# Optimization experiments

Measured on AMD Instinct MI355X. Metric: run time of the kernel, lower is better.

## Reference

```python
import jax, jax.numpy as jnp
import numpy as np
from jax import lax

B, N, C = 8, 16384, 96
ROPE_BASE = 10000.0


def _rope(x):
    """Faithful port of the module's RoPE. x: (b, h, w, c).
    Note: the original computes angles over the h axis but, due to torch
    broadcasting of (h, k_max) against (b, h, w, k_max), the rotation is
    applied along the w axis (valid since h == w)."""
    b, h, w, c = x.shape
    k_max = c // 2
    theta = 1.0 / (ROPE_BASE ** (jnp.arange(k_max, dtype=x.dtype) / k_max))  # (k_max,)
    angles = jnp.arange(h, dtype=x.dtype)[:, None] * theta                  # (h, k_max)
    cos = jnp.cos(angles)[None, None, :, :]  # broadcast over w axis
    sin = jnp.sin(angles)[None, None, :, :]
    xr = x.reshape(b, h, w, k_max, 2)
    xre, xim = xr[..., 0], xr[..., 1]
    ore = xre * cos - xim * sin
    oim = xre * sin + xim * cos
    return jnp.stack([ore, oim], axis=-1).reshape(b, h, w, c)


def setup_inputs() -> dict:
    key = jax.random.key(0)
    ks = jax.random.split(key, 5)
    return {
        "x": jax.random.normal(ks[0], (B, N, C), dtype=jnp.float32),
        "qk_w": jax.random.normal(ks[1], (2 * C, C), dtype=jnp.float32) * 0.05,
        "qk_b": jax.random.normal(ks[2], (2 * C,), dtype=jnp.float32) * 0.02,
        "lepe_w": jax.random.normal(ks[3], (C, 1, 3, 3), dtype=jnp.float32) * 0.1,
        "lepe_b": jax.random.normal(ks[4], (C,), dtype=jnp.float32) * 0.02,
        "num_heads": 4,
    }


def reference(x, qk_w, qk_b, lepe_w, lepe_b, num_heads):
    b, n, c = x.shape
    h = w = int(round(n ** 0.5))
    d = c // num_heads
    inv_sqrt_n = float(n) ** (-0.5)

    qk = x @ qk_w.T + qk_b                        # (b, n, 2c)
    q = jax.nn.elu(qk[..., :c]) + 1.0             # (b, n, c)
    k = jax.nn.elu(qk[..., c:]) + 1.0
    v = x

    q_rope = _rope(q.reshape(b, h, w, c)).reshape(b, n, num_heads, d).transpose(0, 2, 1, 3)
    k_rope = _rope(k.reshape(b, h, w, c)).reshape(b, n, num_heads, d).transpose(0, 2, 1, 3)
    qh = q.reshape(b, n, num_heads, d).transpose(0, 2, 1, 3)  # (b, H, n, d)
    kh = k.reshape(b, n, num_heads, d).transpose(0, 2, 1, 3)
    vh = v.reshape(b, n, num_heads, d).transpose(0, 2, 1, 3)

    k_mean = kh.mean(axis=2, keepdims=True)                         # (b, H, 1, d)
    z = 1.0 / (jnp.einsum('bhnd,bhmd->bhnm', qh, k_mean) + 1e-6)    # (b, H, n, 1)
    kv = jnp.einsum('bhnd,bhne->bhde', k_rope * inv_sqrt_n, vh * inv_sqrt_n)  # (b, H, d, d)
    out = jnp.einsum('bhnd,bhde->bhne', q_rope, kv) * z             # (b, H, n, d)
    out = out.transpose(0, 2, 1, 3).reshape(b, n, c)

    # LePE: depthwise 3x3 conv on v laid out as (b, c, h, w)
    v_img = vh.transpose(0, 2, 1, 3).reshape(b, h, w, c).transpose(0, 3, 1, 2)
    lepe = lax.conv_general_dilated(
        v_img, lepe_w, window_strides=(1, 1), padding='SAME',
        feature_group_count=c, dimension_numbers=('NCHW', 'OIHW', 'NCHW'))
    lepe = lepe + lepe_b[None, :, None, None]
    return out + lepe.transpose(0, 2, 3, 1).reshape(b, n, c)
```

## Files before the change

kernel.cpp:

```cpp
#include <hip/hip_runtime.h>


#define NLINE 16384
#define CCH 96
#define KTP 136
#define QSP 104
#define OUTP 98
#define THETA_COEF 0.2768273412406135f
#define LOG2_2PI   2.6514961294723187f

typedef __attribute__((ext_vector_type(4))) float f32x4;
typedef __attribute__((ext_vector_type(8))) short bf16x8;
typedef __attribute__((ext_vector_type(2))) __fp16 fp16x2;

__device__ __forceinline__ unsigned short f2bf(float f) {
  unsigned int u = __float_as_uint(f);
  u += 0x7FFFu + ((u >> 16) & 1u);
  return (unsigned short)(u >> 16);
}
__device__ __forceinline__ float bf2f(unsigned short h) {
  return __uint_as_float(((unsigned int)h) << 16);
}
__device__ __forceinline__ bf16x8 pack_bf8(f32x4 v0, f32x4 v1) {
  bf16x8 r;
  r[0] = (short)f2bf(v0.x); r[1] = (short)f2bf(v0.y);
  r[2] = (short)f2bf(v0.z); r[3] = (short)f2bf(v0.w);
  r[4] = (short)f2bf(v1.x); r[5] = (short)f2bf(v1.y);
  r[6] = (short)f2bf(v1.z); r[7] = (short)f2bf(v1.w);
  return r;
}

__global__ void prep_w2(const float* __restrict__ qkw,
                        unsigned short* __restrict__ wfrag,
                        float* __restrict__ kv_g) {
  int idx = blockIdx.x * 256 + threadIdx.x;
  if (idx < 19200) kv_g[idx] = 0.0f;
  if (idx < 2304) {
    int u = idx;
    int lane = u & 63;
    int nt = (u >> 6) % 6;
    int rest = u / 384;
    int kk = rest % 3, half = rest / 3;
    int lr = lane & 15, q4 = lane >> 4;
    const float* src = qkw + (half * 96 + nt * 16 + lr) * 96 + kk * 32 + q4 * 8;
    unsigned short* dst = wfrag + (size_t)u * 8;
#pragma unroll
    for (int j = 0; j < 8; ++j) dst[j] = f2bf(src[j]);
  }
}

__global__ __launch_bounds__(256, 4) void la_k1(
    const float* __restrict__ x, const unsigned short* __restrict__ wfrag,
    const float* __restrict__ qkb, float* __restrict__ kv_g,
    float* __restrict__ ksum_g)
{
  const int tid  = threadIdx.x;
  const int b    = blockIdx.x >> 7;
  const int tile = blockIdx.x & 127;

  __shared__ alignas(16) unsigned short kqt[96 * KTP];
  __shared__ float ksum_s[96];

  if (tid < 96) ksum_s[tid] = 0.0f;
  __syncthreads();

  const int wave = tid >> 6;
  const int lane = tid & 63;
  const int lr   = lane & 15;
  const int q4   = lane >> 4;
  const int row0 = wave * 32;
  const float* xb = x + ((size_t)b * NLINE + (size_t)tile * 128) * CCH;

  bf16x8 afr[2][3];
#pragma unroll
  for (int mt = 0; mt < 2; ++mt)
#pragma unroll
    for (int kk = 0; kk < 3; ++kk) {
      const float* ap = xb + (row0 + mt * 16 + lr) * CCH + kk * 32 + q4 * 8;
      afr[mt][kk] = pack_bf8(((const f32x4*)ap)[0], ((const f32x4*)ap)[1]);
    }

  float biasv[6];
#pragma unroll
  for (int nt = 0; nt < 6; ++nt) biasv[nt] = qkb[96 + nt * 16 + lr];

  f32x4 acc[2][6];
#pragma unroll
  for (int mt = 0; mt < 2; ++mt)
#pragma unroll
    for (int nt = 0; nt < 6; ++nt) acc[mt][nt] = (f32x4){0.f, 0.f, 0.f, 0.f};

#pragma unroll
  for (int kk = 0; kk < 3; ++kk) {
#pragma unroll
    for (int nt = 0; nt < 6; ++nt) {
      bf16x8 bf = *(const bf16x8*)&wfrag[(size_t)(((3 + kk) * 6 + nt) * 64 + lane) * 8];
      acc[0][nt] = __builtin_amdgcn_mfma_f32_16x16x32_bf16(afr[0][kk], bf, acc[0][nt], 0, 0, 0);
      acc[1][nt] = __builtin_amdgcn_mfma_f32_16x16x32_bf16(afr[1][kk], bf, acc[1][nt], 0, 0, 0);
    }
  }

  const int odd = lr & 1;
#pragma unroll
  for (int nt = 0; nt < 6; ++nt) {
    const int col = nt * 16 + lr;
    const float threv = exp2f(-THETA_COEF * (float)(col >> 1) - LOG2_2PI);
    float csum = 0.0f;
    float vv[2][4];
#pragma unroll
    for (int mt = 0; mt < 2; ++mt)
#pragma unroll
      for (int rg = 0; rg < 4; ++rg) {
        float v = acc[mt][nt][rg] + biasv[nt];
        v = (v > 0.0f) ? (v + 1.0f) : __expf(v);
        csum += v;
        vv[mt][rg] = v;
      }
    atomicAdd(&ksum_s[col], csum);
#pragma unroll
    for (int mt = 0; mt < 2; ++mt) {
      unsigned long long pk = 0;
#pragma unroll
      for (int rg = 0; rg < 4; ++rg) {
        float p = __shfl_xor(vv[mt][rg], 1);
        int r = row0 + mt * 16 + q4 * 4 + rg;
        float rev = (float)r * threv;
        float sn = __builtin_amdgcn_sinf(rev);
        float cn = __builtin_amdgcn_cosf(rev);
        float o = odd ? (p * sn + vv[mt][rg] * cn)
                      : (vv[mt][rg] * cn - p * sn);
        pk |= (unsigned long long)f2bf(o) << (16 * rg);
      }
      *(unsigned long long*)&kqt[col * KTP + row0 + mt * 16 + q4 * 4] = pk;
    }
  }
  __syncthreads();

  if (tid < 96) atomicAdd(&ksum_g[b * 96 + tid], ksum_s[tid]);

  const int h = wave;
  f32x4 kvacc[2][2];
#pragma unroll
  for (int mt = 0; mt < 2; ++mt)
#pragma unroll
    for (int nt = 0; nt < 2; ++nt) kvacc[mt][nt] = (f32x4){0.f, 0.f, 0.f, 0.f};

#pragma unroll
  for (int kk = 0; kk < 4; ++kk) {
    const int rbase = kk * 32 + q4 * 8;
    bf16x8 ka[2], vb[2];
#pragma unroll
    for (int mt = 0; mt < 2; ++mt) {
      int c = 24 * h + mt * 16 + lr; if (c > 95) c = 95;
      ka[mt] = *(const bf16x8*)&kqt[c * KTP + rbase];
    }
#pragma unroll
    for (int nt = 0; nt < 2; ++nt) {
      int c = 24 * h + nt * 16 + lr; if (c > 95) c = 95;
#pragma unroll
      for (int j = 0; j < 8; ++j)
        vb[nt][j] = (short)f2bf(xb[(rbase + j) * CCH + c]);
    }
#pragma unroll
    for (int mt = 0; mt < 2; ++mt)
#pragma unroll
      for (int nt = 0; nt < 2; ++nt)
        kvacc[mt][nt] = __builtin_amdgcn_mfma_f32_16x16x32_bf16(ka[mt], vb[nt], kvacc[mt][nt], 0, 0, 0);
  }

  const float inv_n = 1.0f / 16384.0f;
  float* kvb = kv_g + ((size_t)b * 4 + h) * 576;
#pragma unroll
  for (int mt = 0; mt < 2; ++mt)
#pragma unroll
    for (int rg = 0; rg < 4; ++rg) {
      int d = mt * 16 + q4 * 4 + rg;
      if (d < 24) {
#pragma unroll
        for (int nt = 0; nt < 2; ++nt) {
          int e = nt * 16 + lr;
          if (e < 24) atomicAdd(&kvb[d * 24 + e], kvacc[mt][nt][rg] * inv_n);
        }
      }
    }
}

__global__ __launch_bounds__(256, 8) void la_k2(
    const float* __restrict__ x, const unsigned short* __restrict__ wfrag,
    const float* __restrict__ qkb, const float* __restrict__ lepe_w,
    const float* __restrict__ lepe_b, const float* __restrict__ kv_g,
    const float* __restrict__ ksum_g, float* __restrict__ out)
{
  const int tid = threadIdx.x;
  const int b   = blockIdx.x & 7;
  const int seg = blockIdx.x >> 3;
  const int y   = seg >> 1;

  __shared__ alignas(16) unsigned short qs[64 * QSP];
  __shared__ alignas(16) float zs[64 * 4];
  __shared__ float lepe_s[9 * 96];

  for (int i = tid; i < 864; i += 256) {
    int ch = i / 9, tap = i % 9;
    lepe_s[tap * 96 + (ch & 3) * 24 + (ch >> 2)] = lepe_w[i];
  }

  const int wave = tid >> 6;
  const int lane = tid & 63;
  const int lr   = lane & 15;
  const int q4   = lane >> 4;

  float biasv[6], kmv[6];
#pragma unroll
  for (int nt = 0; nt < 6; ++nt) {
    biasv[nt] = qkb[nt * 16 + lr];
    kmv[nt]   = ksum_g[b * 96 + nt * 16 + lr];
  }

  const float* xb = x + ((size_t)b * NLINE + (size_t)seg * 64) * CCH;
  bf16x8 afrag[3];
#pragma unroll
  for (int kk = 0; kk < 3; ++kk) {
    const float* ap = xb + (wave * 16 + lr) * CCH + kk * 32 + q4 * 8;
    afrag[kk] = pack_bf8(((const f32x4*)ap)[0], ((const f32x4*)ap)[1]);
  }

  f32x4 acc[6];
#pragma unroll
  for (int nt = 0; nt < 6; ++nt) acc[nt] = (f32x4){0.f, 0.f, 0.f, 0.f};
#pragma unroll
  for (int kk = 0; kk < 3; ++kk) {
#pragma unroll
    for (int nt = 0; nt < 6; ++nt) {
      bf16x8 bf = *(const bf16x8*)&wfrag[(size_t)((kk * 6 + nt) * 64 + lane) * 8];
      acc[nt] = __builtin_amdgcn_mfma_f32_16x16x32_bf16(afrag[kk], bf, acc[nt], 0, 0, 0);
    }
  }

  const int odd = lr & 1;
  const int t0  = wave * 16 + q4 * 4;
  const int xwb = ((seg & 1) << 6) + t0;
  float d0[4], d1[4], d2[4], d3[4];
#pragma unroll
  for (int rg = 0; rg < 4; ++rg) { d0[rg] = 0.f; d1[rg] = 0.f; d2[rg] = 0.f; d3[rg] = 0.f; }

#pragma unroll
  for (int nt = 0; nt < 6; ++nt) {
    const int col = nt * 16 + lr;
    const float threv = exp2f(-THETA_COEF * (float)(col >> 1) - LOG2_2PI);
    float vv[4];
#pragma unroll
    for (int rg = 0; rg < 4; ++rg) {
      float v = acc[nt][rg] + biasv[nt];
      v = (v > 0.0f) ? (v + 1.0f) : __expf(v);
      vv[rg] = v;
    }
#pragma unroll
    for (int rg = 0; rg < 4; ++rg) {
      float p = vv[rg] * kmv[nt];
      if (nt == 0)      d0[rg] += p;
      else if (nt == 1) { if (lr < 8) d0[rg] += p; else d1[rg] += p; }
      else if (nt == 2) d1[rg] += p;
      else if (nt == 3) d2[rg] += p;
      else if (nt == 4) { if (lr < 8) d2[rg] += p; else d3[rg] += p; }
      else              d3[rg] += p;
    }
#pragma unroll
    for (int rg = 0; rg < 4; ++rg) {
      float p = __shfl_xor(vv[rg], 1);
      float rev = (float)(xwb + rg) * threv;
      float sn = __builtin_amdgcn_sinf(rev);
      float cn = __builtin_amdgcn_cosf(rev);
      float o = odd ? (p * sn + vv[rg] * cn)
                    : (vv[rg] * cn - p * sn);
      qs[(t0 + rg) * QSP + col] = f2bf(o);
    }
  }

  {
    const float inv_n = 1.0f / 16384.0f;
#pragma unroll
    for (int rg = 0; rg < 4; ++rg) {
      float s0 = d0[rg], s1 = d1[rg], s2 = d2[rg], s3 = d3[rg];
#pragma unroll
      for (int m = 1; m <= 8; m <<= 1) {
        s0 += __shfl_xor(s0, m);
        s1 += __shfl_xor(s1, m);
        s2 += __shfl_xor(s2, m);
        s3 += __shfl_xor(s3, m);
      }
      if (lr == 0) {
        f32x4 zv = { 1.0f / (s0 * inv_n + 1e-6f), 1.0f / (s1 * inv_n + 1e-6f),
                     1.0f / (s2 * inv_n + 1e-6f), 1.0f / (s3 * inv_n + 1e-6f) };
        *(f32x4*)&zs[(t0 + rg) * 4] = zv;
      }
    }
  }
  __syncthreads();

  const int h2 = wave;
  bf16x8 qa[4];
#pragma unroll
  for (int m = 0; m < 4; ++m) {
    qa[m] = *(const bf16x8*)&qs[(16 * m + lr) * QSP + 24 * h2 + q4 * 8];
    if (q4 == 3) {
#pragma unroll
      for (int j = 0; j < 8; ++j) qa[m][j] = 0;
    }
  }
  bf16x8 kb[2];
  {
    const float* kvh = kv_g + ((size_t)b * 4 + h2) * 576;
#pragma unroll
    for (int n = 0; n < 2; ++n)
#pragma unroll
      for (int j = 0; j < 8; ++j) {
        int d = q4 * 8 + j, e = n * 16 + lr;
        kb[n][j] = (d < 24 && e < 24) ? (short)f2bf(kvh[d * 24 + e]) : (short)0;
      }
  }
  f32x4 c2[4][2];
#pragma unroll
  for (int m = 0; m < 4; ++m)
#pragma unroll
    for (int n = 0; n < 2; ++n) c2[m][n] = (f32x4){0.f, 0.f, 0.f, 0.f};
#pragma unroll
  for (int m = 0; m < 4; ++m)
#pragma unroll
    for (int n = 0; n < 2; ++n)
      c2[m][n] = __builtin_amdgcn_mfma_f32_16x16x32_bf16(qa[m], kb[n], c2[m][n], 0, 0, 0);

  __syncthreads();

  __fp16* outs = (__fp16*)qs;
  {
    float lb0 = lepe_b[24 * h2 + lr];
    float lb1 = (lr < 8) ? lepe_b[24 * h2 + 16 + lr] : 0.0f;
#pragma unroll
    for (int m = 0; m < 4; ++m)
#pragma unroll
      for (int rg = 0; rg < 4; ++rg) {
        int t = 16 * m + q4 * 4 + rg;
        float zv = zs[t * 4 + h2];
        outs[t * OUTP + 24 * h2 + lr] = (__fp16)(c2[m][0][rg] * zv + lb0);
        if (lr < 8)
          outs[t * OUTP + 24 * h2 + 16 + lr] = (__fp16)(c2[m][1][rg] * zv + lb1);
      }
  }
  __syncthreads();

  float* ob = out + ((size_t)b * NLINE + (size_t)seg * 64) * CCH;
  const float* xg = x + (size_t)b * NLINE * CCH;
#pragma unroll
  for (int k = 0; k < 6; ++k) {
    int idx = tid + 256 * k;
    int tl = idx / 24, c4 = idx % 24;
    int ch0 = c4 * 4;
    int xw = ((seg & 1) << 6) + tl;

    fp16x2 p0 = *(const fp16x2*)&outs[tl * OUTP + ch0];
    fp16x2 p1 = *(const fp16x2*)&outs[tl * OUTP + ch0 + 2];
    float r0 = (float)p0[0], r1 = (float)p0[1];
    float r2 = (float)p1[0], r3 = (float)p1[1];

#pragma unroll
    for (int dy = 0; dy < 3; ++dy) {
      int yy = y + dy - 1;
      if (yy < 0 || yy > 127) continue;
      const float* rowp = xg + ((size_t)yy * 128) * CCH;
#pragma unroll
      for (int dx = 0; dx < 3; ++dx) {
        int xx = xw + dx - 1;
        if (xx < 0 || xx > 127) continue;
        f32x4 v = *(const f32x4*)(rowp + xx * CCH + ch0);
        const float* wp = &lepe_s[(dy * 3 + dx) * 96 + c4];
        r0 += wp[0]  * v.x;
        r1 += wp[24] * v.y;
        r2 += wp[48] * v.z;
        r3 += wp[72] * v.w;
      }
    }
    f32x4 o = { r0, r1, r2, r3 };
    ((f32x4*)ob)[idx] = o;
  }
}

extern "C" void kernel_launch(void* const* d_in, const int* in_sizes, int n_in,
                              void* d_out, int out_size, void* d_ws, size_t ws_size,
                              hipStream_t stream) {
  const float* x      = (const float*)d_in[0];
  const float* qkw    = (const float*)d_in[1];
  const float* qkb    = (const float*)d_in[2];
  const float* lepe_w = (const float*)d_in[3];
  const float* lepe_b = (const float*)d_in[4];
  float* out = (float*)d_out;

  unsigned short* wfrag = (unsigned short*)d_ws;
  float* kv_g   = (float*)((char*)d_ws + 36864);
  float* ksum_g = kv_g + 18432;

  prep_w2<<<dim3(75), dim3(256), 0, stream>>>(qkw, wfrag, kv_g);
  la_k1<<<dim3(1024), dim3(256), 0, stream>>>(x, wfrag, qkb, kv_g, ksum_g);
  la_k2<<<dim3(2048), dim3(256), 0, stream>>>(x, wfrag, qkb, lepe_w, lepe_b,
                                              kv_g, ksum_g, out);
}
```

Before: 175.5 us.

## Halve k1 tile to 64 rows, transpose kv layout, vectorize LePE weights

The first kernel now processes 64-row tiles instead of 128, launches twice as many blocks, and raises the occupancy hint. This gives more parallelism and halves the LDS footprint. The kv accumulator is stored transposed and padded to 32 so the second kernel can load kv fragments with vector loads instead of scalar gathers. LePE weights are stored in natural channel order so they can be fetched with a single float4 LDS read. The trade-off is twice as many global atomics on kv and ksum from the extra blocks.

```diff
diff --git a/kernel.cpp b/kernel.cpp
--- a/kernel.cpp
+++ b/kernel.cpp
@@ -3,7 +3,7 @@
 
 #define NLINE 16384
 #define CCH 96
-#define KTP 136
+#define KTP 72
 #define QSP 104
 #define OUTP 98
 #define THETA_COEF 0.2768273412406135f
@@ -34,7 +34,7 @@
                         unsigned short* __restrict__ wfrag,
                         float* __restrict__ kv_g) {
   int idx = blockIdx.x * 256 + threadIdx.x;
-  if (idx < 19200) kv_g[idx] = 0.0f;
+  if (idx < 25344) kv_g[idx] = 0.0f;
   if (idx < 2304) {
     int u = idx;
     int lane = u & 63;
@@ -49,14 +49,15 @@
   }
 }
 
-__global__ __launch_bounds__(256, 4) void la_k1(
+__global__ __launch_bounds__(256, 8) void la_k1(
     const float* __restrict__ x, const unsigned short* __restrict__ wfrag,
     const float* __restrict__ qkb, float* __restrict__ kv_g,
     float* __restrict__ ksum_g)
 {
   const int tid  = threadIdx.x;
-  const int b    = blockIdx.x >> 7;
-  const int tile = blockIdx.x & 127;
+  const int b    = blockIdx.x & 7;
+  const int seg  = blockIdx.x >> 3;
+  const int half = seg & 1;
 
   __shared__ alignas(16) unsigned short kqt[96 * KTP];
   __shared__ float ksum_s[96];
@@ -64,39 +65,32 @@
   if (tid < 96) ksum_s[tid] = 0.0f;
   __syncthreads();
 
-  const int wave = tid >> 6;
+  const int wv   = tid >> 6;
   const int lane = tid & 63;
   const int lr   = lane & 15;
   const int q4   = lane >> 4;
-  const int row0 = wave * 32;
-  const float* xb = x + ((size_t)b * NLINE + (size_t)tile * 128) * CCH;
-
-  bf16x8 afr[2][3];
-#pragma unroll
-  for (int mt = 0; mt < 2; ++mt)
-#pragma unroll
-    for (int kk = 0; kk < 3; ++kk) {
-      const float* ap = xb + (row0 + mt * 16 + lr) * CCH + kk * 32 + q4 * 8;
-      afr[mt][kk] = pack_bf8(((const f32x4*)ap)[0], ((const f32x4*)ap)[1]);
-    }
+  const float* xb = x + ((size_t)b * NLINE + (size_t)seg * 64) * CCH;
+
+  bf16x8 afr[3];
+#pragma unroll
+  for (int kk = 0; kk < 3; ++kk) {
+    const float* ap = xb + (wv * 16 + lr) * CCH + kk * 32 + q4 * 8;
+    afr[kk] = pack_bf8(((const f32x4*)ap)[0], ((const f32x4*)ap)[1]);
+  }
 
   float biasv[6];
 #pragma unroll
   for (int nt = 0; nt < 6; ++nt) biasv[nt] = qkb[96 + nt * 16 + lr];
 
-  f32x4 acc[2][6];
-#pragma unroll
-  for (int mt = 0; mt < 2; ++mt)
-#pragma unroll
-    for (int nt = 0; nt < 6; ++nt) acc[mt][nt] = (f32x4){0.f, 0.f, 0.f, 0.f};
-
+  f32x4 acc[6];
+#pragma unroll
+  for (int nt = 0; nt < 6; ++nt) acc[nt] = (f32x4){0.f, 0.f, 0.f, 0.f};
 #pragma unroll
   for (int kk = 0; kk < 3; ++kk) {
 #pragma unroll
     for (int nt = 0; nt < 6; ++nt) {
       bf16x8 bf = *(const bf16x8*)&wfrag[(size_t)(((3 + kk) * 6 + nt) * 64 + lane) * 8];
-      acc[0][nt] = __builtin_amdgcn_mfma_f32_16x16x32_bf16(afr[0][kk], bf, acc[0][nt], 0, 0, 0);
-      acc[1][nt] = __builtin_amdgcn_mfma_f32_16x16x32_bf16(afr[1][kk], bf, acc[1][nt], 0, 0, 0);
+      acc[nt] = __builtin_amdgcn_mfma_f32_16x16x32_bf16(afr[kk], bf, acc[nt], 0, 0, 0);
     }
   }
 
@@ -106,39 +100,34 @@
     const int col = nt * 16 + lr;
     const float threv = exp2f(-THETA_COEF * (float)(col >> 1) - LOG2_2PI);
     float csum = 0.0f;
-    float vv[2][4];
-#pragma unroll
-    for (int mt = 0; mt < 2; ++mt)
-#pragma unroll
-      for (int rg = 0; rg < 4; ++rg) {
-        float v = acc[mt][nt][rg] + biasv[nt];
-        v = (v > 0.0f) ? (v + 1.0f) : __expf(v);
-        csum += v;
-        vv[mt][rg] = v;
-      }
+    float vv[4];
+#pragma unroll
+    for (int rg = 0; rg < 4; ++rg) {
+      float v = acc[nt][rg] + biasv[nt];
+      v = (v > 0.0f) ? (v + 1.0f) : __expf(v);
+      csum += v;
+      vv[rg] = v;
+    }
     atomicAdd(&ksum_s[col], csum);
-#pragma unroll
-    for (int mt = 0; mt < 2; ++mt) {
-      unsigned long long pk = 0;
-#pragma unroll
-      for (int rg = 0; rg < 4; ++rg) {
-        float p = __shfl_xor(vv[mt][rg], 1);
-        int r = row0 + mt * 16 + q4 * 4 + rg;
-        float rev = (float)r * threv;
-        float sn = __builtin_amdgcn_sinf(rev);
-        float cn = __builtin_amdgcn_cosf(rev);
-        float o = odd ? (p * sn + vv[mt][rg] * cn)
-                      : (vv[mt][rg] * cn - p * sn);
-        pk |= (unsigned long long)f2bf(o) << (16 * rg);
-      }
-      *(unsigned long long*)&kqt[col * KTP + row0 + mt * 16 + q4 * 4] = pk;
-    }
+    unsigned long long pk = 0;
+#pragma unroll
+    for (int rg = 0; rg < 4; ++rg) {
+      float p = __shfl_xor(vv[rg], 1);
+      int r = half * 64 + wv * 16 + q4 * 4 + rg;
+      float rev = (float)r * threv;
+      float sn = __builtin_amdgcn_sinf(rev);
+      float cn = __builtin_amdgcn_cosf(rev);
+      float o = odd ? (p * sn + vv[rg] * cn)
+                    : (vv[rg] * cn - p * sn);
+      pk |= (unsigned long long)f2bf(o) << (16 * rg);
+    }
+    *(unsigned long long*)&kqt[col * KTP + wv * 16 + q4 * 4] = pk;
   }
   __syncthreads();
 
   if (tid < 96) atomicAdd(&ksum_g[b * 96 + tid], ksum_s[tid]);
 
-  const int h = wave;
+  const int h = wv;
   f32x4 kvacc[2][2];
 #pragma unroll
   for (int mt = 0; mt < 2; ++mt)
@@ -146,7 +135,7 @@
     for (int nt = 0; nt < 2; ++nt) kvacc[mt][nt] = (f32x4){0.f, 0.f, 0.f, 0.f};
 
 #pragma unroll
-  for (int kk = 0; kk < 4; ++kk) {
+  for (int kk = 0; kk < 2; ++kk) {
     const int rbase = kk * 32 + q4 * 8;
     bf16x8 ka[2], vb[2];
 #pragma unroll
@@ -169,7 +158,7 @@
   }
 
   const float inv_n = 1.0f / 16384.0f;
-  float* kvb = kv_g + ((size_t)b * 4 + h) * 576;
+  float* kvbT = kv_g + ((size_t)b * 4 + h) * 768;
 #pragma unroll
   for (int mt = 0; mt < 2; ++mt)
 #pragma unroll
@@ -179,7 +168,7 @@
 #pragma unroll
         for (int nt = 0; nt < 2; ++nt) {
           int e = nt * 16 + lr;
-          if (e < 24) atomicAdd(&kvb[d * 24 + e], kvacc[mt][nt][rg] * inv_n);
+          if (e < 24) atomicAdd(&kvbT[e * 32 + d], kvacc[mt][nt][rg] * inv_n);
         }
       }
     }
@@ -198,11 +187,11 @@
 
   __shared__ alignas(16) unsigned short qs[64 * QSP];
   __shared__ alignas(16) float zs[64 * 4];
-  __shared__ float lepe_s[9 * 96];
+  __shared__ alignas(16) float lepe_s[9 * 96];
 
   for (int i = tid; i < 864; i += 256) {
     int ch = i / 9, tap = i % 9;
-    lepe_s[tap * 96 + (ch & 3) * 24 + (ch >> 2)] = lepe_w[i];
+    lepe_s[tap * 96 + ch] = lepe_w[i];
   }
 
   const int wave = tid >> 6;
@@ -310,14 +299,14 @@
   }
   bf16x8 kb[2];
   {
-    const float* kvh = kv_g + ((size_t)b * 4 + h2) * 576;
-#pragma unroll
-    for (int n = 0; n < 2; ++n)
-#pragma unroll
-      for (int j = 0; j < 8; ++j) {
-        int d = q4 * 8 + j, e = n * 16 + lr;
-        kb[n][j] = (d < 24 && e < 24) ? (short)f2bf(kvh[d * 24 + e]) : (short)0;
-      }
+    const float* kvhT = kv_g + ((size_t)b * 4 + h2) * 768;
+#pragma unroll
+    for (int n = 0; n < 2; ++n) {
+      int e = n * 16 + lr;
+      int er = (e < 24) ? e : 0;
+      const f32x4* p = (const f32x4*)&kvhT[er * 32 + q4 * 8];
+      kb[n] = pack_bf8(p[0], p[1]);
+    }
   }
   f32x4 c2[4][2];
 #pragma unroll
@@ -373,11 +362,11 @@
         int xx = xw + dx - 1;
         if (xx < 0 || xx > 127) continue;
         f32x4 v = *(const f32x4*)(rowp + xx * CCH + ch0);
-        const float* wp = &lepe_s[(dy * 3 + dx) * 96 + c4];
-        r0 += wp[0]  * v.x;
-        r1 += wp[24] * v.y;
-        r2 += wp[48] * v.z;
-        r3 += wp[72] * v.w;
+        f32x4 w = *(const f32x4*)&lepe_s[(dy * 3 + dx) * 96 + ch0];
+        r0 += w.x * v.x;
+        r1 += w.y * v.y;
+        r2 += w.z * v.z;
+        r3 += w.w * v.w;
       }
     }
     f32x4 o = { r0, r1, r2, r3 };
@@ -397,10 +386,10 @@
 
   unsigned short* wfrag = (unsigned short*)d_ws;
   float* kv_g   = (float*)((char*)d_ws + 36864);
-  float* ksum_g = kv_g + 18432;
-
-  prep_w2<<<dim3(75), dim3(256), 0, stream>>>(qkw, wfrag, kv_g);
-  la_k1<<<dim3(1024), dim3(256), 0, stream>>>(x, wfrag, qkb, kv_g, ksum_g);
+  float* ksum_g = kv_g + 24576;
+
+  prep_w2<<<dim3(100), dim3(256), 0, stream>>>(qkw, wfrag, kv_g);
+  la_k1<<<dim3(2048), dim3(256), 0, stream>>>(x, wfrag, qkb, kv_g, ksum_g);
   la_k2<<<dim3(2048), dim3(256), 0, stream>>>(x, wfrag, qkb, lepe_w, lepe_b,
                                               kv_g, ksum_g, out);
 }
```

New measurement: 228.7 us. 30.3% more time.

## Replace global atomics for kv/ksum with per-tile partials and a reduce kernel

Applied to the files above, without the earlier changes.

When the workspace is large enough, each la_k1 block writes its kv and ksum partial sums to its own slot in memory, and a new la_reduce kernel sums the 128 tiles per batch. This replaces heavy atomic contention on a small global buffer. The kv matrix is now stored transposed and padded so la_k2 can load B fragments with vector loads. The LePE weights are reordered so each tap is read with one vector load. The change adds a kernel launch and about 9 MB of partial traffic, and it depends on ws_size to pick a path.

```diff
diff --git a/kernel.cpp b/kernel.cpp
--- a/kernel.cpp
+++ b/kernel.cpp
@@ -32,9 +32,9 @@
 
 __global__ void prep_w2(const float* __restrict__ qkw,
                         unsigned short* __restrict__ wfrag,
-                        float* __restrict__ kv_g) {
+                        float* __restrict__ kvT) {
   int idx = blockIdx.x * 256 + threadIdx.x;
-  if (idx < 19200) kv_g[idx] = 0.0f;
+  if (idx < 25344) kvT[idx] = 0.0f;
   if (idx < 2304) {
     int u = idx;
     int lane = u & 63;
@@ -51,8 +51,9 @@
 
 __global__ __launch_bounds__(256, 4) void la_k1(
     const float* __restrict__ x, const unsigned short* __restrict__ wfrag,
-    const float* __restrict__ qkb, float* __restrict__ kv_g,
-    float* __restrict__ ksum_g)
+    const float* __restrict__ qkb, float* __restrict__ kvT,
+    float* __restrict__ ksum_g, float* __restrict__ kvp,
+    float* __restrict__ ksump)
 {
   const int tid  = threadIdx.x;
   const int b    = blockIdx.x >> 7;
@@ -136,7 +137,10 @@
   }
   __syncthreads();
 
-  if (tid < 96) atomicAdd(&ksum_g[b * 96 + tid], ksum_s[tid]);
+  if (tid < 96) {
+    if (kvp) ksump[((size_t)b * 128 + tile) * 96 + tid] = ksum_s[tid];
+    else     atomicAdd(&ksum_g[b * 96 + tid], ksum_s[tid]);
+  }
 
   const int h = wave;
   f32x4 kvacc[2][2];
@@ -168,27 +172,79 @@
         kvacc[mt][nt] = __builtin_amdgcn_mfma_f32_16x16x32_bf16(ka[mt], vb[nt], kvacc[mt][nt], 0, 0, 0);
   }
 
-  const float inv_n = 1.0f / 16384.0f;
-  float* kvb = kv_g + ((size_t)b * 4 + h) * 576;
-#pragma unroll
-  for (int mt = 0; mt < 2; ++mt)
-#pragma unroll
-    for (int rg = 0; rg < 4; ++rg) {
-      int d = mt * 16 + q4 * 4 + rg;
-      if (d < 24) {
-#pragma unroll
-        for (int nt = 0; nt < 2; ++nt) {
-          int e = nt * 16 + lr;
-          if (e < 24) atomicAdd(&kvb[d * 24 + e], kvacc[mt][nt][rg] * inv_n);
+  if (kvp) {
+    float* dst = kvp + ((size_t)(b * 128 + tile) * 4 + h) * 576;
+#pragma unroll
+    for (int mt = 0; mt < 2; ++mt)
+#pragma unroll
+      for (int rg = 0; rg < 4; ++rg) {
+        int d = mt * 16 + q4 * 4 + rg;
+        if (d < 24) {
+#pragma unroll
+          for (int nt = 0; nt < 2; ++nt) {
+            int e = nt * 16 + lr;
+            if (e < 24) dst[d * 24 + e] = kvacc[mt][nt][rg];
+          }
         }
       }
-    }
+  } else {
+    const float inv_n = 1.0f / 16384.0f;
+    float* kvbT = kvT + ((size_t)b * 4 + h) * 768;
+#pragma unroll
+    for (int mt = 0; mt < 2; ++mt)
+#pragma unroll
+      for (int rg = 0; rg < 4; ++rg) {
+        int d = mt * 16 + q4 * 4 + rg;
+        if (d < 24) {
+#pragma unroll
+          for (int nt = 0; nt < 2; ++nt) {
+            int e = nt * 16 + lr;
+            if (e < 24) atomicAdd(&kvbT[e * 32 + d], kvacc[mt][nt][rg] * inv_n);
+          }
+        }
+      }
+  }
+}
+
+__global__ void la_reduce(const float* __restrict__ kvp,
+                          const float* __restrict__ ksump,
+                          float* __restrict__ kvT,
+                          float* __restrict__ ksum_g) {
+  int i = blockIdx.x * 256 + threadIdx.x;
+  if (i < 18432) {
+    int bh = i / 576, de = i - bh * 576;
+    int b = bh >> 2, h = bh & 3;
+    int d = de / 24, e = de - d * 24;
+    const float* src = kvp + ((size_t)b * 512 + h) * 576 + de;
+    float s0 = 0.f, s1 = 0.f, s2 = 0.f, s3 = 0.f;
+#pragma unroll 4
+    for (int p = 0; p < 128; p += 4) {
+      s0 += src[(p + 0) * 2304];
+      s1 += src[(p + 1) * 2304];
+      s2 += src[(p + 2) * 2304];
+      s3 += src[(p + 3) * 2304];
+    }
+    kvT[(size_t)bh * 768 + e * 32 + d] = ((s0 + s1) + (s2 + s3)) * (1.0f / 16384.0f);
+  } else if (i < 19200) {
+    int j = i - 18432;
+    int b = j / 96, c = j - b * 96;
+    const float* src = ksump + (size_t)b * 128 * 96 + c;
+    float s0 = 0.f, s1 = 0.f, s2 = 0.f, s3 = 0.f;
+#pragma unroll 4
+    for (int p = 0; p < 128; p += 4) {
+      s0 += src[(p + 0) * 96];
+      s1 += src[(p + 1) * 96];
+      s2 += src[(p + 2) * 96];
+      s3 += src[(p + 3) * 96];
+    }
+    ksum_g[b * 96 + c] = (s0 + s1) + (s2 + s3);
+  }
 }
 
 __global__ __launch_bounds__(256, 8) void la_k2(
     const float* __restrict__ x, const unsigned short* __restrict__ wfrag,
     const float* __restrict__ qkb, const float* __restrict__ lepe_w,
-    const float* __restrict__ lepe_b, const float* __restrict__ kv_g,
+    const float* __restrict__ lepe_b, const float* __restrict__ kvT,
     const float* __restrict__ ksum_g, float* __restrict__ out)
 {
   const int tid = threadIdx.x;
@@ -198,11 +254,11 @@
 
   __shared__ alignas(16) unsigned short qs[64 * QSP];
   __shared__ alignas(16) float zs[64 * 4];
-  __shared__ float lepe_s[9 * 96];
+  __shared__ alignas(16) float lepe_s[9 * 96];
 
   for (int i = tid; i < 864; i += 256) {
     int ch = i / 9, tap = i % 9;
-    lepe_s[tap * 96 + (ch & 3) * 24 + (ch >> 2)] = lepe_w[i];
+    lepe_s[tap * 96 + ch] = lepe_w[i];
   }
 
   const int wave = tid >> 6;
@@ -310,14 +366,14 @@
   }
   bf16x8 kb[2];
   {
-    const float* kvh = kv_g + ((size_t)b * 4 + h2) * 576;
-#pragma unroll
-    for (int n = 0; n < 2; ++n)
-#pragma unroll
-      for (int j = 0; j < 8; ++j) {
-        int d = q4 * 8 + j, e = n * 16 + lr;
-        kb[n][j] = (d < 24 && e < 24) ? (short)f2bf(kvh[d * 24 + e]) : (short)0;
-      }
+    const float* kvhT = kvT + ((size_t)b * 4 + h2) * 768;
+#pragma unroll
+    for (int n = 0; n < 2; ++n) {
+      int e = n * 16 + lr;
+      int er = (e < 24) ? e : 0;
+      const f32x4* p = (const f32x4*)&kvhT[er * 32 + q4 * 8];
+      kb[n] = pack_bf8(p[0], p[1]);
+    }
   }
   f32x4 c2[4][2];
 #pragma unroll
@@ -373,11 +429,11 @@
         int xx = xw + dx - 1;
         if (xx < 0 || xx > 127) continue;
         f32x4 v = *(const f32x4*)(rowp + xx * CCH + ch0);
-        const float* wp = &lepe_s[(dy * 3 + dx) * 96 + c4];
-        r0 += wp[0]  * v.x;
-        r1 += wp[24] * v.y;
-        r2 += wp[48] * v.z;
-        r3 += wp[72] * v.w;
+        f32x4 w = *(const f32x4*)&lepe_s[(dy * 3 + dx) * 96 + ch0];
+        r0 += w.x * v.x;
+        r1 += w.y * v.y;
+        r2 += w.z * v.z;
+        r3 += w.w * v.w;
       }
     }
     f32x4 o = { r0, r1, r2, r3 };
@@ -396,11 +452,19 @@
   float* out = (float*)d_out;
 
   unsigned short* wfrag = (unsigned short*)d_ws;
-  float* kv_g   = (float*)((char*)d_ws + 36864);
-  float* ksum_g = kv_g + 18432;
-
-  prep_w2<<<dim3(75), dim3(256), 0, stream>>>(qkw, wfrag, kv_g);
-  la_k1<<<dim3(1024), dim3(256), 0, stream>>>(x, wfrag, qkb, kv_g, ksum_g);
+  float* kvT    = (float*)((char*)d_ws + 36864);
+  float* ksum_g = kvT + 24576;
+  float* kvp    = ksum_g + 768;
+  float* ksump  = kvp + 2359296;
+
+  const bool partial = (ws_size >= 9968640u);
+
+  prep_w2<<<dim3(100), dim3(256), 0, stream>>>(qkw, wfrag, kvT);
+  la_k1<<<dim3(1024), dim3(256), 0, stream>>>(x, wfrag, qkb, kvT, ksum_g,
+                                              partial ? kvp : nullptr,
+                                              partial ? ksump : nullptr);
+  if (partial)
+    la_reduce<<<dim3(75), dim3(256), 0, stream>>>(kvp, ksump, kvT, ksum_g);
   la_k2<<<dim3(2048), dim3(256), 0, stream>>>(x, wfrag, qkb, lepe_w, lepe_b,
-                                              kv_g, ksum_g, out);
-}
+                                              kvT, ksum_g, out);
+}
```

New measurement: 170.9 us. 1.03x faster.
